# Performance work log

Hardware: AMD Instinct MI355X
Metric: run time of the kernel (lower is better)

## Reference

```python
import jax, jax.numpy as jnp
import numpy as np
import math

B, N, C = 8, 4096, 768
H = 12
DH = C // H
M = 256
LN_EPS = 1e-5


def setup_inputs() -> dict:
    key = jax.random.key(0)
    ks = jax.random.split(key, 7)
    x = jax.random.normal(ks[0], (B, N, C), dtype=jnp.float32)
    # torch Linear weight [out,in]; store transposed for y = x @ W
    W_qkv = jax.random.normal(ks[1], (C, 3 * C), dtype=jnp.float32) * (1.0 / math.sqrt(C))
    W_proj = jax.random.normal(ks[2], (C, C), dtype=jnp.float32) * (1.0 / math.sqrt(C))
    b_proj = jnp.zeros((C,), dtype=jnp.float32)
    gamma = jnp.ones((C,), dtype=jnp.float32)
    beta = jnp.zeros((C,), dtype=jnp.float32)
    random_features = jax.random.normal(ks[3], (M, DH), dtype=jnp.float32) / math.sqrt(DH)
    return {"x": x, "W_qkv": W_qkv, "W_proj": W_proj, "b_proj": b_proj,
            "gamma": gamma, "beta": beta, "random_features": random_features}


def _phi(t, random_features):
    # t: [B, H, N, DH] -> [B, H, N, M]; phi(x) = exp(w·x - ||x||^2/2) / sqrt(M)
    norm_sq = 0.5 * jnp.sum(t * t, axis=-1, keepdims=True)
    proj = jnp.einsum('bhnd,md->bhnm', t, random_features)
    return jnp.exp(proj - norm_sq) * (1.0 / math.sqrt(M))


def reference(x, W_qkv, W_proj, b_proj, gamma, beta, random_features):
    b, n, c = x.shape
    qkv = (x @ W_qkv).reshape(b, n, 3, H, DH)
    qkv = jnp.transpose(qkv, (2, 0, 3, 1, 4))  # [3, B, H, N, DH]
    q, k, v = qkv[0], qkv[1], qkv[2]

    q_p = _phi(q, random_features)  # [B,H,N,M]
    k_p = _phi(k, random_features)  # [B,H,N,M]

    kv = jnp.einsum('bhnm,bhnd->bhmd', k_p, v)       # [B,H,M,DH]
    out = jnp.einsum('bhnm,bhmd->bhnd', q_p, kv)     # [B,H,N,DH]

    k_sum = jnp.sum(k_p, axis=2)                      # [B,H,M]
    normalizer = jnp.einsum('bhnm,bhm->bhn', q_p, k_sum)[..., None]
    out = out / (normalizer + 1e-6)

    x_attn = jnp.transpose(out, (0, 2, 1, 3)).reshape(b, n, c)
    x_attn = x_attn @ W_proj + b_proj
    # dropout is identity in eval / p=0

    y = x + x_attn
    mu = jnp.mean(y, axis=-1, keepdims=True)
    var = jnp.mean(jnp.square(y - mu), axis=-1, keepdims=True)
    return (y - mu) * jax.lax.rsqrt(var + LN_EPS) * gamma + beta
```

## Files before the change

kernel.cpp:

```cpp
#include <hip/hip_runtime.h>
#include <hip/hip_fp16.h>


#define LOG2E 1.44269504088896340736f

typedef _Float16 half8 __attribute__((ext_vector_type(8)));
typedef _Float16 half4_t __attribute__((ext_vector_type(4)));
typedef _Float16 half2_t __attribute__((ext_vector_type(2)));
typedef float f32x4 __attribute__((ext_vector_type(4)));

#if __has_builtin(__builtin_amdgcn_fdot2)
#define FDOT2(a, b, c) __builtin_amdgcn_fdot2((a), (b), (c), false)
#else
#define FDOT2(a, b, c) \
  ((float)(a)[0] * (float)(b)[0] + ((float)(a)[1] * (float)(b)[1] + (c)))
#endif

static __device__ __forceinline__ half2_t pk2(float a, float b) {
#if __has_builtin(__builtin_amdgcn_cvt_pkrtz)
  return __builtin_bit_cast(half2_t, __builtin_amdgcn_cvt_pkrtz(a, b));
#else
  half2_t r; r[0] = (_Float16)a; r[1] = (_Float16)b; return r;
#endif
}

__device__ __forceinline__ void glds16(const _Float16* g, _Float16* s) {
  __builtin_amdgcn_global_load_lds(
      (const __attribute__((address_space(1))) void*)g,
      (__attribute__((address_space(3))) unsigned int*)s,
      16, 0, 0);
}


__global__ __launch_bounds__(256)
void prep(const float* __restrict__ x, const float* __restrict__ Wqkv,
          const float* __restrict__ Wproj, const float* __restrict__ rfm,
          _Float16* __restrict__ x_h, _Float16* __restrict__ wqkvT,
          _Float16* __restrict__ wprojT, _Float16* __restrict__ rfh) {
  const long bid = blockIdx.x;
  if (bid < 24576) {
    long i = (bid * 256 + threadIdx.x) * 4;
    float4 v = *(const float4*)(x + i);
    half4_t h;
    h[0] = (_Float16)v.x; h[1] = (_Float16)v.y; h[2] = (_Float16)v.z; h[3] = (_Float16)v.w;
    *(half4_t*)(x_h + i) = h;
    return;
  }
  long idx = (bid - 24576) * 256 + threadIdx.x;
  if (idx < 1769472) {
    int k = (int)(idx / 2304), n = (int)(idx % 2304);
    wqkvT[(long)n * 768 + k] = (_Float16)Wqkv[idx];
  } else if ((idx -= 1769472) < 589824) {
    int k = (int)(idx / 768), n = (int)(idx % 768);
    wprojT[(long)n * 768 + k] = (_Float16)Wproj[idx];
  } else if ((idx -= 589824) < 16384) {
    rfh[idx] = (_Float16)rfm[idx];
  }
}


__device__ __forceinline__ void stage_unit(const _Float16* __restrict__ G, int grow0,
                                           int kcol, _Float16* lds, int w, int l) {
#pragma unroll
  for (int j = 0; j < 2; ++j) {
    const int ci = w + j * 8;
    const int row = ci * 8 + (l >> 3);
    const int col8 = (l & 7) ^ (row & 7);
    glds16(G + (long)(grow0 + row) * 768 + kcol + col8 * 8, lds + ci * 512);
  }
}

static __device__ __forceinline__ half8 ldsw(const _Float16* buf, int r, int sl) {
  return *(const half8*)(buf + r * 64 + ((sl ^ (r & 7)) << 3));
}

__global__ __launch_bounds__(512)
void gemm_qkv(const _Float16* __restrict__ W, const _Float16* __restrict__ X,
              _Float16* __restrict__ qh, _Float16* __restrict__ kh,
              _Float16* __restrict__ vT,
              float* __restrict__ nsqLq, float* __restrict__ nsqLk) {
  __shared__ __align__(16) _Float16 As[32768];
  __shared__ __align__(16) _Float16 Bs[32768];
  const int tid = threadIdx.x;
  const int w = tid >> 6, l = tid & 63;
  const int lr = l & 15, kg = l >> 4;
  const int wr = w >> 2, wc = w & 3;

  const int bid = blockIdx.x;
  const int wg = (bid & 7) * 144 + (bid >> 3);
  const int m0 = (wg % 9) * 256;
  const int n0 = (wg / 9) * 256;

  stage_unit(W, m0,       0,  As,         w, l);
  stage_unit(X, n0,       0,  Bs,         w, l);
  stage_unit(X, n0 + 128, 0,  Bs + 8192,  w, l);
  stage_unit(W, m0 + 128, 0,  As + 8192,  w, l);
  stage_unit(W, m0,       64, As + 16384, w, l);
  stage_unit(X, n0,       64, Bs + 16384, w, l);
  stage_unit(X, n0 + 128, 64, Bs + 24576, w, l);
  asm volatile("s_waitcnt vmcnt(6)" ::: "memory");
  __builtin_amdgcn_s_barrier();

  f32x4 acc[8][4];
#pragma unroll
  for (int t = 0; t < 8; ++t)
#pragma unroll
    for (int u = 0; u < 4; ++u) acc[t][u] = (f32x4){0.f, 0.f, 0.f, 0.f};

  for (int kt = 0; kt < 12; ++kt) {
    const int c = kt & 1, o = c ^ 1;
    const _Float16* Ac = As + c * 16384;
    const _Float16* Bc = Bs + c * 16384;
    half8 aR[4][2], bR0[2][2], bR1[2][2];

#pragma unroll
    for (int i = 0; i < 4; ++i) {
      const int r = wr * 16 + i * 32 + lr;
      aR[i][0] = ldsw(Ac, r, kg);
      aR[i][1] = ldsw(Ac, r, 4 + kg);
    }
#pragma unroll
    for (int j = 0; j < 2; ++j) {
      const int r = wc * 16 + j * 64 + lr;
      bR0[j][0] = ldsw(Bc, r, kg);
      bR0[j][1] = ldsw(Bc, r, 4 + kg);
    }
    if (kt + 1 < 12)
      stage_unit(W, m0 + 128, (kt + 1) * 64, As + o * 16384 + 8192, w, l);
    __builtin_amdgcn_s_barrier();
    __builtin_amdgcn_s_setprio(1);
#pragma unroll
    for (int ks = 0; ks < 2; ++ks)
#pragma unroll
      for (int i = 0; i < 4; ++i)
#pragma unroll
        for (int j = 0; j < 2; ++j)
          acc[i][j] = __builtin_amdgcn_mfma_f32_16x16x32_f16(aR[i][ks], bR0[j][ks],
                                                             acc[i][j], 0, 0, 0);
    __builtin_amdgcn_s_setprio(0);
    __builtin_amdgcn_s_barrier();

#pragma unroll
    for (int j = 0; j < 2; ++j) {
      const int r = 128 + wc * 16 + j * 64 + lr;
      bR1[j][0] = ldsw(Bc, r, kg);
      bR1[j][1] = ldsw(Bc, r, 4 + kg);
    }
    if (kt + 2 < 12)
      stage_unit(W, m0, (kt + 2) * 64, As + c * 16384, w, l);
    __builtin_amdgcn_s_barrier();
    __builtin_amdgcn_s_setprio(1);
#pragma unroll
    for (int ks = 0; ks < 2; ++ks)
#pragma unroll
      for (int i = 0; i < 4; ++i)
#pragma unroll
        for (int j = 0; j < 2; ++j)
          acc[i][2 + j] = __builtin_amdgcn_mfma_f32_16x16x32_f16(aR[i][ks], bR1[j][ks],
                                                                 acc[i][2 + j], 0, 0, 0);
    __builtin_amdgcn_s_setprio(0);
    __builtin_amdgcn_s_barrier();

#pragma unroll
    for (int i = 0; i < 4; ++i) {
      const int r = 128 + wr * 16 + i * 32 + lr;
      aR[i][0] = ldsw(Ac, r, kg);
      aR[i][1] = ldsw(Ac, r, 4 + kg);
    }
    if (kt + 2 < 12)
      stage_unit(X, n0, (kt + 2) * 64, Bs + c * 16384, w, l);
    __builtin_amdgcn_s_barrier();
    __builtin_amdgcn_s_setprio(1);
#pragma unroll
    for (int ks = 0; ks < 2; ++ks)
#pragma unroll
      for (int i = 0; i < 4; ++i)
#pragma unroll
        for (int j = 0; j < 2; ++j)
          acc[4 + i][2 + j] = __builtin_amdgcn_mfma_f32_16x16x32_f16(aR[i][ks], bR1[j][ks],
                                                                     acc[4 + i][2 + j], 0, 0, 0);
    __builtin_amdgcn_s_setprio(0);
    __builtin_amdgcn_s_barrier();

    if (kt + 2 < 12)
      stage_unit(X, n0 + 128, (kt + 2) * 64, Bs + c * 16384 + 8192, w, l);
    if (kt < 10)
      asm volatile("s_waitcnt vmcnt(6)" ::: "memory");
    else
      asm volatile("s_waitcnt vmcnt(0)" ::: "memory");
    __builtin_amdgcn_s_barrier();
    __builtin_amdgcn_s_setprio(1);
#pragma unroll
    for (int ks = 0; ks < 2; ++ks)
#pragma unroll
      for (int i = 0; i < 4; ++i)
#pragma unroll
        for (int j = 0; j < 2; ++j)
          acc[4 + i][j] = __builtin_amdgcn_mfma_f32_16x16x32_f16(aR[i][ks], bR0[j][ks],
                                                                 acc[4 + i][j], 0, 0, 0);
    __builtin_amdgcn_s_setprio(0);
    __builtin_amdgcn_s_barrier();
  }

  const int which = (m0 >= 1536) ? 2 : ((m0 >= 768) ? 1 : 0);
  const int hbase = (m0 - which * 768) >> 6;
  const int b_ = n0 >> 12;
  const int nb = n0 & 4095;

  if (which < 2) {
    _Float16* dst = which ? kh : qh;
    float* nd = which ? nsqLk : nsqLq;
    float ns[4][4];
#pragma unroll
    for (int a = 0; a < 4; ++a)
#pragma unroll
      for (int b2 = 0; b2 < 4; ++b2) ns[a][b2] = 0.f;
#pragma unroll
    for (int t = 0; t < 8; ++t) {
      const int h = hbase + (t >> 1);
      const int d0 = wr * 16 + (t & 1) * 32 + kg * 4;
#pragma unroll
      for (int u = 0; u < 4; ++u) {
        const int n_ = nb + wc * 16 + u * 64 + lr;
        half2_t h01 = pk2(acc[t][u][0], acc[t][u][1]);
        half2_t h23 = pk2(acc[t][u][2], acc[t][u][3]);
        half4_t p4; p4[0] = h01[0]; p4[1] = h01[1]; p4[2] = h23[0]; p4[3] = h23[1];
        *(half4_t*)(dst + ((long)(b_ * 12 + h) * 4096 + n_) * 64 + d0) = p4;
#pragma unroll
        for (int r = 0; r < 4; ++r) { float f = (float)p4[r]; ns[t >> 1][u] += f * f; }
      }
    }
    float* nsP = (float*)As;
#pragma unroll
    for (int h2 = 0; h2 < 4; ++h2)
#pragma unroll
      for (int u = 0; u < 4; ++u) {
        float s = ns[h2][u];
        s += __shfl_xor(s, 16);
        s += __shfl_xor(s, 32);
        if (kg == 0) nsP[wr * 1024 + h2 * 256 + wc * 16 + u * 64 + lr] = s;
      }
    __syncthreads();
#pragma unroll
    for (int e = 0; e < 2; ++e) {
      const int idx = tid + e * 512;
      const int h2 = idx >> 8, tk = idx & 255;
      const float vsum = nsP[h2 * 256 + tk] + nsP[1024 + h2 * 256 + tk];
      nd[(long)(b_ * 12 + hbase + h2) * 4096 + nb + tk] = 0.5f * vsum * LOG2E + 4.0f;
    }
  } else {
#pragma unroll
    for (int t = 0; t < 8; ++t) {
      const int h = hbase + (t >> 1);
      const long hb = (long)(b_ * 12 + h) * 64;
      const int d0 = wr * 16 + (t & 1) * 32 + kg * 4;
#pragma unroll
      for (int u = 0; u < 4; ++u) {
        const int n_ = nb + wc * 16 + u * 64 + lr;
#pragma unroll
        for (int r = 0; r < 4; ++r)
          vT[(hb + d0 + r) * 4096 + n_] = (_Float16)acc[t][u][r];
      }
    }
  }
}


__global__ __launch_bounds__(256)
void gemm_proj(const _Float16* __restrict__ A, const _Float16* __restrict__ BT,
               float* __restrict__ Co, const float* __restrict__ bias,
               const float* __restrict__ resid) {
  __shared__ __align__(16) _Float16 As[128 * 32];
  __shared__ __align__(16) _Float16 Bs[128 * 32];
  const int tid = threadIdx.x;
  const int w = tid >> 6, l = tid & 63;
  const int lr = l & 15, kg = l >> 4;
  const int m0 = blockIdx.y * 128;
  const int n0 = blockIdx.x * 128;
  const int wm = (w >> 1) * 64, wn = (w & 1) * 64;

  const _Float16* gA = A + (long)(m0 + w * 32 + (l >> 2)) * 768 + (l & 3) * 8;
  const _Float16* gB = BT + (long)(n0 + w * 32 + (l >> 2)) * 768 + (l & 3) * 8;
  _Float16* sA = As + (w * 32) * 32;
  _Float16* sB = Bs + (w * 32) * 32;

  f32x4 acc[4][4];
#pragma unroll
  for (int t = 0; t < 4; ++t)
#pragma unroll
    for (int u = 0; u < 4; ++u) acc[t][u] = (f32x4){0.f, 0.f, 0.f, 0.f};

  for (int kc = 0; kc < 24; ++kc) {
    __syncthreads();
    glds16(gA, sA);
    glds16(gA + 16 * 768, sA + 16 * 32);
    glds16(gB, sB);
    glds16(gB + 16 * 768, sB + 16 * 32);
    gA += 32; gB += 32;
    __syncthreads();

    half8 af[4], bf[4];
#pragma unroll
    for (int t = 0; t < 4; ++t)
      af[t] = *(const half8*)(As + (wm + t * 16 + lr) * 32 + kg * 8);
#pragma unroll
    for (int u = 0; u < 4; ++u)
      bf[u] = *(const half8*)(Bs + (wn + u * 16 + lr) * 32 + kg * 8);
#pragma unroll
    for (int t = 0; t < 4; ++t)
#pragma unroll
      for (int u = 0; u < 4; ++u)
        acc[t][u] = __builtin_amdgcn_mfma_f32_16x16x32_f16(af[t], bf[u], acc[t][u], 0, 0, 0);
  }

#pragma unroll
  for (int u = 0; u < 4; ++u) {
    const int col = n0 + wn + u * 16 + lr;
    const float bv = bias[col];
#pragma unroll
    for (int t = 0; t < 4; ++t) {
      const int row = m0 + wm + t * 16 + kg * 4;
#pragma unroll
      for (int r = 0; r < 4; ++r) {
        long idx = (long)(row + r) * 768 + col;
        Co[idx] = acc[t][u][r] + bv + resid[idx];
      }
    }
  }
}


__global__ __launch_bounds__(256)
void kv_fused(const _Float16* __restrict__ kh, const _Float16* __restrict__ vT,
              const _Float16* __restrict__ rfh, const float* __restrict__ nsqLk,
              _Float16* __restrict__ kvpart, float* __restrict__ kspart) {
  __shared__ __align__(16) _Float16 Ka[64 * 32], Kb[64 * 32];
  __shared__ __align__(16) _Float16 Va[64 * 32], Vb[64 * 32];
  __shared__ __align__(16) _Float16 P[256 * 72];
  const int chunk = blockIdx.x, bh = blockIdx.y;
  const int tid = threadIdx.x, w = tid >> 6, l = tid & 63;
  const int lr = l & 15, kg = l >> 4;
  const long khbase = (long)bh * 4096 * 64;
  const long vtbase = (long)bh * 64 * 4096;
  const half2_t ONES = {(_Float16)1.f, (_Float16)1.f};

  half8 rf[4][2];
#pragma unroll
  for (int u = 0; u < 4; ++u)
#pragma unroll
    for (int ks = 0; ks < 2; ++ks)
      rf[u][ks] = *(const half8*)(rfh + (w * 64 + u * 16 + lr) * 64 + ks * 32 + kg * 8);

  f32x4 kvacc[4][4];
#pragma unroll
  for (int mt = 0; mt < 4; ++mt)
#pragma unroll
    for (int dt = 0; dt < 4; ++dt) kvacc[mt][dt] = (f32x4){0.f, 0.f, 0.f, 0.f};
  float ksacc[4] = {0.f, 0.f, 0.f, 0.f};

  for (int t8 = 0; t8 < 8; ++t8) {
    const int nt = chunk * 512 + t8 * 64;
    __syncthreads();
    if (w == 0) {
#pragma unroll
      for (int j = 0; j < 4; ++j)
        glds16(kh + khbase + (long)(nt + j * 16 + (l >> 2)) * 64 + (l & 3) * 8, Ka + j * 512);
    } else if (w == 1) {
#pragma unroll
      for (int j = 0; j < 4; ++j)
        glds16(kh + khbase + (long)(nt + j * 16 + (l >> 2)) * 64 + 32 + (l & 3) * 8, Kb + j * 512);
    } else if (w == 2) {
#pragma unroll
      for (int j = 0; j < 4; ++j)
        glds16(vT + vtbase + (long)(j * 16 + (l >> 2)) * 4096 + nt + (l & 3) * 8, Va + j * 512);
    } else {
#pragma unroll
      for (int j = 0; j < 4; ++j)
        glds16(vT + vtbase + (long)(j * 16 + (l >> 2)) * 4096 + nt + 32 + (l & 3) * 8, Vb + j * 512);
    }
    __syncthreads();

    half8 af[4][2];
#pragma unroll
    for (int tt = 0; tt < 4; ++tt) {
      af[tt][0] = *(const half8*)(Ka + (tt * 16 + lr) * 32 + kg * 8);
      af[tt][1] = *(const half8*)(Kb + (tt * 16 + lr) * 32 + kg * 8);
    }
    f32x4 sacc[4][4];
#pragma unroll
    for (int tt = 0; tt < 4; ++tt)
#pragma unroll
      for (int u = 0; u < 4; ++u) sacc[tt][u] = (f32x4){0.f, 0.f, 0.f, 0.f};
#pragma unroll
    for (int ks = 0; ks < 2; ++ks)
#pragma unroll
      for (int tt = 0; tt < 4; ++tt)
#pragma unroll
        for (int u = 0; u < 4; ++u)
          sacc[tt][u] = __builtin_amdgcn_mfma_f32_16x16x32_f16(af[tt][ks], rf[u][ks],
                                                               sacc[tt][u], 0, 0, 0);
    float4 nsq4[4];
#pragma unroll
    for (int tt = 0; tt < 4; ++tt)
      nsq4[tt] = *(const float4*)(nsqLk + (long)bh * 4096 + nt + tt * 16 + kg * 4);
#pragma unroll
    for (int tt = 0; tt < 4; ++tt)
#pragma unroll
      for (int u = 0; u < 4; ++u) {
        float e0 = exp2f(sacc[tt][u][0] * LOG2E - nsq4[tt].x);
        float e1 = exp2f(sacc[tt][u][1] * LOG2E - nsq4[tt].y);
        float e2 = exp2f(sacc[tt][u][2] * LOG2E - nsq4[tt].z);
        float e3 = exp2f(sacc[tt][u][3] * LOG2E - nsq4[tt].w);
        half2_t h01 = pk2(e0, e1), h23 = pk2(e2, e3);
        half4_t p4; p4[0] = h01[0]; p4[1] = h01[1]; p4[2] = h23[0]; p4[3] = h23[1];
        *(half4_t*)(P + (w * 64 + u * 16 + lr) * 72 + tt * 16 + kg * 4) = p4;
      }
#pragma unroll
    for (int ks = 0; ks < 2; ++ks) {
      half8 pa[4], bv[4];
#pragma unroll
      for (int mt = 0; mt < 4; ++mt)
        pa[mt] = *(const half8*)(P + (w * 64 + mt * 16 + lr) * 72 + ks * 32 + kg * 8);
#pragma unroll
      for (int dt = 0; dt < 4; ++dt)
        bv[dt] = *(const half8*)((ks == 0 ? Va : Vb) + (dt * 16 + lr) * 32 + kg * 8);
#pragma unroll
      for (int mt = 0; mt < 4; ++mt)
#pragma unroll
        for (int dt = 0; dt < 4; ++dt)
          kvacc[mt][dt] = __builtin_amdgcn_mfma_f32_16x16x32_f16(pa[mt], bv[dt],
                                                                 kvacc[mt][dt], 0, 0, 0);
#pragma unroll
      for (int mt = 0; mt < 4; ++mt) {
        const half2_t* pp = (const half2_t*)&pa[mt];
#pragma unroll
        for (int p = 0; p < 4; ++p) ksacc[mt] = FDOT2(pp[p], ONES, ksacc[mt]);
      }
    }
  }

#pragma unroll
  for (int mt = 0; mt < 4; ++mt) {
    float v = ksacc[mt];
    v += __shfl_xor(v, 16);
    v += __shfl_xor(v, 32);
    if (l < 16) kspart[((bh * 8 + chunk) << 8) + w * 64 + mt * 16 + l] = v;
  }
#pragma unroll
  for (int mt = 0; mt < 4; ++mt)
#pragma unroll
    for (int dt = 0; dt < 4; ++dt)
#pragma unroll
      for (int r = 0; r < 4; ++r)
        kvpart[(((long)(bh * 8 + chunk) * 256) + w * 64 + mt * 16 + kg * 4 + r) * 64 +
               dt * 16 + lr] = (_Float16)kvacc[mt][dt][r];
}


__global__ __launch_bounds__(256)
void reduce_all(const _Float16* __restrict__ kvpart, const float* __restrict__ kspart,
                _Float16* __restrict__ kvT, _Float16* __restrict__ ksumh) {
  if (blockIdx.x < 6144) {
    long i = (long)blockIdx.x * 256 + threadIdx.x;
    const int bh = (int)(i >> 14);
    const int rem = (int)(i & 16383);
    const int m = rem >> 6, d = rem & 63;
    float s = 0.f;
#pragma unroll
    for (int c = 0; c < 8; ++c)
      s += (float)kvpart[(((long)bh * 8 + c) * 256 + m) * 64 + d];
    kvT[(long)bh * 16384 + d * 256 + m] = (_Float16)s;
  } else {
    int i = (blockIdx.x - 6144) * 256 + threadIdx.x;
    int bh = i >> 8, m = i & 255;
    float s = 0.f;
#pragma unroll
    for (int c = 0; c < 8; ++c) s += kspart[((bh * 8 + c) << 8) + m];
    ksumh[i] = (_Float16)s;
  }
}


__global__ __launch_bounds__(256)
void attn_fused(const _Float16* __restrict__ qh, const _Float16* __restrict__ rfh,
                const float* __restrict__ nsqLq, const _Float16* __restrict__ kvT,
                const _Float16* __restrict__ ksumh, _Float16* __restrict__ attn) {
  __shared__ __align__(16) _Float16 Qa[64 * 32], Qb[64 * 32];
  __shared__ __align__(16) _Float16 KV[64 * 264];
  __shared__ __align__(16) _Float16 KS[256];
  __shared__ __align__(16) _Float16 P[64 * 264];
  __shared__ __align__(16) float NS[64];
  const int chunk = blockIdx.x, bh = blockIdx.y;
  const int b = bh / 12, h = bh % 12;
  const int tid = threadIdx.x, w = tid >> 6, l = tid & 63;
  const int lr = l & 15, kg = l >> 4;

  {
    const int d = tid >> 2, mb = (tid & 3) * 64;
#pragma unroll
    for (int j = 0; j < 8; ++j)
      *(half8*)(KV + d * 264 + mb + j * 8) =
          *(const half8*)(kvT + (long)bh * 16384 + d * 256 + mb + j * 8);
    if (tid < 32) *(half8*)(KS + tid * 8) = *(const half8*)(ksumh + bh * 256 + tid * 8);
  }

  half8 rf[4][2];
#pragma unroll
  for (int mt = 0; mt < 4; ++mt)
#pragma unroll
    for (int ks = 0; ks < 2; ++ks)
      rf[mt][ks] = *(const half8*)(rfh + (w * 64 + mt * 16 + lr) * 64 + ks * 32 + kg * 8);

  for (int t8 = 0; t8 < 4; ++t8) {
    const int nt = chunk * 256 + t8 * 64;
    __syncthreads();
    if (w == 0) {
#pragma unroll
      for (int j = 0; j < 4; ++j)
        glds16(qh + ((long)bh * 4096 + nt + j * 16 + (l >> 2)) * 64 + (l & 3) * 8, Qa + j * 512);
    } else if (w == 1) {
#pragma unroll
      for (int j = 0; j < 4; ++j)
        glds16(qh + ((long)bh * 4096 + nt + j * 16 + (l >> 2)) * 64 + 32 + (l & 3) * 8, Qb + j * 512);
    }
    __syncthreads();

    half8 bq[4][2];
#pragma unroll
    for (int tt = 0; tt < 4; ++tt) {
      bq[tt][0] = *(const half8*)(Qa + (tt * 16 + lr) * 32 + kg * 8);
      bq[tt][1] = *(const half8*)(Qb + (tt * 16 + lr) * 32 + kg * 8);
    }
    f32x4 sacc[4][4];
#pragma unroll
    for (int mt = 0; mt < 4; ++mt)
#pragma unroll
      for (int tt = 0; tt < 4; ++tt) sacc[mt][tt] = (f32x4){0.f, 0.f, 0.f, 0.f};
#pragma unroll
    for (int ks = 0; ks < 2; ++ks)
#pragma unroll
      for (int mt = 0; mt < 4; ++mt)
#pragma unroll
        for (int tt = 0; tt < 4; ++tt)
          sacc[mt][tt] = __builtin_amdgcn_mfma_f32_16x16x32_f16(rf[mt][ks], bq[tt][ks],
                                                                sacc[mt][tt], 0, 0, 0);
    float nsqv[4];
#pragma unroll
    for (int tt = 0; tt < 4; ++tt)
      nsqv[tt] = nsqLq[(long)bh * 4096 + nt + tt * 16 + lr];
#pragma unroll
    for (int mt = 0; mt < 4; ++mt)
#pragma unroll
      for (int tt = 0; tt < 4; ++tt) {
        float e0 = exp2f(sacc[mt][tt][0] * LOG2E - nsqv[tt]);
        float e1 = exp2f(sacc[mt][tt][1] * LOG2E - nsqv[tt]);
        float e2 = exp2f(sacc[mt][tt][2] * LOG2E - nsqv[tt]);
        float e3 = exp2f(sacc[mt][tt][3] * LOG2E - nsqv[tt]);
        half2_t h01 = pk2(e0, e1), h23 = pk2(e2, e3);
        half4_t p4; p4[0] = h01[0]; p4[1] = h01[1]; p4[2] = h23[0]; p4[3] = h23[1];
        *(half4_t*)(P + (tt * 16 + lr) * 264 + w * 64 + mt * 16 + kg * 4) = p4;
      }
    __syncthreads();

    f32x4 oacc[4];
#pragma unroll
    for (int u = 0; u < 4; ++u) oacc[u] = (f32x4){0.f, 0.f, 0.f, 0.f};
    float nacc = 0.f;
#pragma unroll
    for (int ks = 0; ks < 8; ++ks) {
      half8 ap = *(const half8*)(P + (w * 16 + lr) * 264 + ks * 32 + kg * 8);
      half8 kv8 = *(const half8*)(KS + ks * 32 + kg * 8);
      const half2_t* a2 = (const half2_t*)&ap;
      const half2_t* k2 = (const half2_t*)&kv8;
#pragma unroll
      for (int p = 0; p < 4; ++p) nacc = FDOT2(a2[p], k2[p], nacc);
#pragma unroll
      for (int u = 0; u < 4; ++u) {
        half8 bkv = *(const half8*)(KV + (u * 16 + lr) * 264 + ks * 32 + kg * 8);
        oacc[u] = __builtin_amdgcn_mfma_f32_16x16x32_f16(ap, bkv, oacc[u], 0, 0, 0);
      }
    }
    nacc += __shfl_xor(nacc, 16);
    nacc += __shfl_xor(nacc, 32);
    if (l < 16) NS[w * 16 + l] = nacc;
    f32x4 n4 = *(const f32x4*)(NS + w * 16 + kg * 4);
    float inv[4];
#pragma unroll
    for (int r = 0; r < 4; ++r) inv[r] = 1.f / (n4[r] + 1e-6f);
#pragma unroll
    for (int u = 0; u < 4; ++u)
#pragma unroll
      for (int r = 0; r < 4; ++r)
        attn[((long)b * 4096 + nt + w * 16 + kg * 4 + r) * 768 + h * 64 + u * 16 + lr] =
            (_Float16)(oacc[u][r] * inv[r]);
  }
}


__global__ __launch_bounds__(256)
void ln_kernel(const float* __restrict__ y, const float* __restrict__ gamma,
               const float* __restrict__ beta, float* __restrict__ outp) {
  const int wv = threadIdx.x >> 6, l = threadIdx.x & 63;
  const long row = (long)blockIdx.x * 4 + wv;
  const float* yr = y + row * 768;
  float v[12];
  float s = 0.f;
#pragma unroll
  for (int j = 0; j < 12; ++j) { v[j] = yr[l + j * 64]; s += v[j]; }
#pragma unroll
  for (int off = 32; off; off >>= 1) s += __shfl_xor(s, off);
  const float mu = s * (1.f / 768.f);
  float vs = 0.f;
#pragma unroll
  for (int j = 0; j < 12; ++j) { float d = v[j] - mu; vs += d * d; }
#pragma unroll
  for (int off = 32; off; off >>= 1) vs += __shfl_xor(vs, off);
  const float rstd = rsqrtf(vs * (1.f / 768.f) + 1e-5f);
  float* orp = outp + row * 768;
#pragma unroll
  for (int j = 0; j < 12; ++j)
    orp[l + j * 64] = (v[j] - mu) * rstd * gamma[l + j * 64] + beta[l + j * 64];
}


extern "C" void kernel_launch(void* const* d_in, const int* in_sizes, int n_in,
                              void* d_out, int out_size, void* d_ws, size_t ws_size,
                              hipStream_t stream) {
  const float* x = (const float*)d_in[0];
  const float* Wqkv = (const float*)d_in[1];
  const float* Wproj = (const float*)d_in[2];
  const float* bproj = (const float*)d_in[3];
  const float* gamma = (const float*)d_in[4];
  const float* beta = (const float*)d_in[5];
  const float* rfm = (const float*)d_in[6];

  char* ws = (char*)d_ws;
  size_t off = 0;
  auto alloc = [&](size_t bytes) -> void* {
    void* p = ws + off;
    off += (bytes + 255) & ~(size_t)255;
    return p;
  };
  char* regionA = (char*)alloc(50331648ULL);
  _Float16* x_h = (_Float16*)regionA;
  _Float16* kvpart = (_Float16*)regionA;
  _Float16* attn = (_Float16*)regionA;

  _Float16* wqkvT = (_Float16*)alloc(1769472ULL * 2);
  _Float16* wprojT = (_Float16*)alloc(589824ULL * 2);
  _Float16* rfh = (_Float16*)alloc(16384ULL * 2);
  _Float16* qh = (_Float16*)alloc(25165824ULL * 2);
  _Float16* kh = (_Float16*)alloc(25165824ULL * 2);
  _Float16* vT = (_Float16*)alloc(25165824ULL * 2);
  float* nsqLq = (float*)alloc(393216ULL * 4);
  float* nsqLk = (float*)alloc(393216ULL * 4);
  float* kspart = (float*)alloc(96ULL * 8 * 256 * 4);
  _Float16* kvT = (_Float16*)alloc(96ULL * 16384 * 2);
  _Float16* ksumh = (_Float16*)alloc(96ULL * 256 * 2);

  float* y = (float*)d_out;

  prep<<<33856, 256, 0, stream>>>(x, Wqkv, Wproj, rfm, x_h, wqkvT, wprojT, rfh);
  gemm_qkv<<<1152, 512, 0, stream>>>(wqkvT, x_h, qh, kh, vT, nsqLq, nsqLk);
  kv_fused<<<dim3(8, 96), 256, 0, stream>>>(kh, vT, rfh, nsqLk, kvpart, kspart);
  reduce_all<<<6240, 256, 0, stream>>>(kvpart, kspart, kvT, ksumh);
  attn_fused<<<dim3(16, 96), 256, 0, stream>>>(qh, rfh, nsqLq, kvT, ksumh, attn);
  gemm_proj<<<dim3(6, 256), 256, 0, stream>>>(attn, wprojT, y, bproj, x);
  ln_kernel<<<8192, 256, 0, stream>>>(y, gamma, beta, y);
}
```

Before: 612.9 us.

## Tile weight transpose through LDS and prefetch next k-tile GEMM fragments

The prep kernel now transposes Wqkv and Wproj in 64x64 tiles through shared memory, giving coalesced float4 reads and half8 writes in place of strided scalar stores, and it launches far fewer blocks. The QKV GEMM main loop is reordered so the A and B fragments for the next k-tile are loaded from the other LDS buffer during the last MFMA phase, and each phase's fragment loads are rearranged. This aims to hide LDS read latency behind MFMA work, at the cost of more live vector registers, which may lower occupancy.

Measured after the change: 648.4 us. +5.8%, slower.

```diff
diff --git a/kernel.cpp b/kernel.cpp
--- a/kernel.cpp
+++ b/kernel.cpp
@@ -37,24 +37,47 @@
           const float* __restrict__ Wproj, const float* __restrict__ rfm,
           _Float16* __restrict__ x_h, _Float16* __restrict__ wqkvT,
           _Float16* __restrict__ wprojT, _Float16* __restrict__ rfh) {
-  const long bid = blockIdx.x;
+  __shared__ _Float16 T[64][72];
+  const int bid = blockIdx.x;
   if (bid < 24576) {
-    long i = (bid * 256 + threadIdx.x) * 4;
+    long i = ((long)bid * 256 + threadIdx.x) * 4;
     float4 v = *(const float4*)(x + i);
     half4_t h;
     h[0] = (_Float16)v.x; h[1] = (_Float16)v.y; h[2] = (_Float16)v.z; h[3] = (_Float16)v.w;
     *(half4_t*)(x_h + i) = h;
     return;
   }
-  long idx = (bid - 24576) * 256 + threadIdx.x;
-  if (idx < 1769472) {
-    int k = (int)(idx / 2304), n = (int)(idx % 2304);
-    wqkvT[(long)n * 768 + k] = (_Float16)Wqkv[idx];
-  } else if ((idx -= 1769472) < 589824) {
-    int k = (int)(idx / 768), n = (int)(idx % 768);
-    wprojT[(long)n * 768 + k] = (_Float16)Wproj[idx];
-  } else if ((idx -= 589824) < 16384) {
-    rfh[idx] = (_Float16)rfm[idx];
+  int tb = bid - 24576;
+  if (tb < 576) {
+    const float* src; _Float16* dst; int Csrc, r0, c0;
+    if (tb < 432) {
+      r0 = (tb / 36) * 64; c0 = (tb % 36) * 64; src = Wqkv; dst = wqkvT; Csrc = 2304;
+    } else {
+      int t2 = tb - 432;
+      r0 = (t2 / 12) * 64; c0 = (t2 % 12) * 64; src = Wproj; dst = wprojT; Csrc = 768;
+    }
+    const int ri = threadIdx.x >> 4;
+    const int ci = (threadIdx.x & 15) * 4;
+#pragma unroll
+    for (int rr = 0; rr < 4; ++rr) {
+      float4 v = *(const float4*)(src + (long)(r0 + ri * 4 + rr) * Csrc + c0 + ci);
+      T[ci + 0][ri * 4 + rr] = (_Float16)v.x;
+      T[ci + 1][ri * 4 + rr] = (_Float16)v.y;
+      T[ci + 2][ri * 4 + rr] = (_Float16)v.z;
+      T[ci + 3][ri * 4 + rr] = (_Float16)v.w;
+    }
+    __syncthreads();
+    const int wi = threadIdx.x >> 3;
+    const int wj = (threadIdx.x & 7) * 8;
+#pragma unroll
+    for (int ww = 0; ww < 2; ++ww) {
+      const int row = wi * 2 + ww;
+      half8 h = *(const half8*)(&T[row][wj]);
+      *(half8*)(dst + (long)(c0 + row) * 768 + r0 + wj) = h;
+    }
+  } else {
+    int idx = (tb - 576) * 256 + threadIdx.x;
+    if (idx < 16384) rfh[idx] = (_Float16)rfm[idx];
   }
 }
 
@@ -107,23 +130,32 @@
 #pragma unroll
     for (int u = 0; u < 4; ++u) acc[t][u] = (f32x4){0.f, 0.f, 0.f, 0.f};
 
+  half8 a0[4][2], a1[4][2], b0[2][2], b1[2][2], b0n[2][2];
+#pragma unroll
+  for (int i = 0; i < 4; ++i) {
+    const int r = wr * 16 + i * 32 + lr;
+    a0[i][0] = ldsw(As, r, kg);
+    a0[i][1] = ldsw(As, r, 4 + kg);
+  }
+#pragma unroll
+  for (int j = 0; j < 2; ++j) {
+    const int r = wc * 16 + j * 64 + lr;
+    b0[j][0] = ldsw(Bs, r, kg);
+    b0[j][1] = ldsw(Bs, r, 4 + kg);
+  }
+
   for (int kt = 0; kt < 12; ++kt) {
     const int c = kt & 1, o = c ^ 1;
     const _Float16* Ac = As + c * 16384;
     const _Float16* Bc = Bs + c * 16384;
-    half8 aR[4][2], bR0[2][2], bR1[2][2];
-
-#pragma unroll
-    for (int i = 0; i < 4; ++i) {
-      const int r = wr * 16 + i * 32 + lr;
-      aR[i][0] = ldsw(Ac, r, kg);
-      aR[i][1] = ldsw(Ac, r, 4 + kg);
-    }
+    const _Float16* An = As + o * 16384;
+    const _Float16* Bn = Bs + o * 16384;
+
 #pragma unroll
     for (int j = 0; j < 2; ++j) {
-      const int r = wc * 16 + j * 64 + lr;
-      bR0[j][0] = ldsw(Bc, r, kg);
-      bR0[j][1] = ldsw(Bc, r, 4 + kg);
+      const int r = 128 + wc * 16 + j * 64 + lr;
+      b1[j][0] = ldsw(Bc, r, kg);
+      b1[j][1] = ldsw(Bc, r, 4 + kg);
     }
     if (kt + 1 < 12)
       stage_unit(W, m0 + 128, (kt + 1) * 64, As + o * 16384 + 8192, w, l);
@@ -135,16 +167,16 @@
       for (int i = 0; i < 4; ++i)
 #pragma unroll
         for (int j = 0; j < 2; ++j)
-          acc[i][j] = __builtin_amdgcn_mfma_f32_16x16x32_f16(aR[i][ks], bR0[j][ks],
+          acc[i][j] = __builtin_amdgcn_mfma_f32_16x16x32_f16(a0[i][ks], b0[j][ks],
                                                              acc[i][j], 0, 0, 0);
     __builtin_amdgcn_s_setprio(0);
     __builtin_amdgcn_s_barrier();
 
 #pragma unroll
-    for (int j = 0; j < 2; ++j) {
-      const int r = 128 + wc * 16 + j * 64 + lr;
-      bR1[j][0] = ldsw(Bc, r, kg);
-      bR1[j][1] = ldsw(Bc, r, 4 + kg);
+    for (int i = 0; i < 4; ++i) {
+      const int r = 128 + wr * 16 + i * 32 + lr;
+      a1[i][0] = ldsw(Ac, r, kg);
+      a1[i][1] = ldsw(Ac, r, 4 + kg);
     }
     if (kt + 2 < 12)
       stage_unit(W, m0, (kt + 2) * 64, As + c * 16384, w, l);
@@ -156,17 +188,11 @@
       for (int i = 0; i < 4; ++i)
 #pragma unroll
         for (int j = 0; j < 2; ++j)
-          acc[i][2 + j] = __builtin_amdgcn_mfma_f32_16x16x32_f16(aR[i][ks], bR1[j][ks],
+          acc[i][2 + j] = __builtin_amdgcn_mfma_f32_16x16x32_f16(a0[i][ks], b1[j][ks],
                                                                  acc[i][2 + j], 0, 0, 0);
     __builtin_amdgcn_s_setprio(0);
     __builtin_amdgcn_s_barrier();
 
-#pragma unroll
-    for (int i = 0; i < 4; ++i) {
-      const int r = 128 + wr * 16 + i * 32 + lr;
-      aR[i][0] = ldsw(Ac, r, kg);
-      aR[i][1] = ldsw(Ac, r, 4 + kg);
-    }
     if (kt + 2 < 12)
       stage_unit(X, n0, (kt + 2) * 64, Bs + c * 16384, w, l);
     __builtin_amdgcn_s_barrier();
@@ -177,7 +203,7 @@
       for (int i = 0; i < 4; ++i)
 #pragma unroll
         for (int j = 0; j < 2; ++j)
-          acc[4 + i][2 + j] = __builtin_amdgcn_mfma_f32_16x16x32_f16(aR[i][ks], bR1[j][ks],
+          acc[4 + i][2 + j] = __builtin_amdgcn_mfma_f32_16x16x32_f16(a1[i][ks], b1[j][ks],
                                                                      acc[4 + i][2 + j], 0, 0, 0);
     __builtin_amdgcn_s_setprio(0);
     __builtin_amdgcn_s_barrier();
@@ -188,6 +214,20 @@
       asm volatile("s_waitcnt vmcnt(6)" ::: "memory");
     else
       asm volatile("s_waitcnt vmcnt(0)" ::: "memory");
+    if (kt + 1 < 12) {
+#pragma unroll
+      for (int i = 0; i < 4; ++i) {
+        const int r = wr * 16 + i * 32 + lr;
+        a0[i][0] = ldsw(An, r, kg);
+        a0[i][1] = ldsw(An, r, 4 + kg);
+      }
+#pragma unroll
+      for (int j = 0; j < 2; ++j) {
+        const int r = wc * 16 + j * 64 + lr;
+        b0n[j][0] = ldsw(Bn, r, kg);
+        b0n[j][1] = ldsw(Bn, r, 4 + kg);
+      }
+    }
     __builtin_amdgcn_s_barrier();
     __builtin_amdgcn_s_setprio(1);
 #pragma unroll
@@ -196,10 +236,14 @@
       for (int i = 0; i < 4; ++i)
 #pragma unroll
         for (int j = 0; j < 2; ++j)
-          acc[4 + i][j] = __builtin_amdgcn_mfma_f32_16x16x32_f16(aR[i][ks], bR0[j][ks],
+          acc[4 + i][j] = __builtin_amdgcn_mfma_f32_16x16x32_f16(a1[i][ks], b0[j][ks],
                                                                  acc[4 + i][j], 0, 0, 0);
     __builtin_amdgcn_s_setprio(0);
     __builtin_amdgcn_s_barrier();
+    if (kt + 1 < 12) {
+#pragma unroll
+      for (int j = 0; j < 2; ++j) { b0[j][0] = b0n[j][0]; b0[j][1] = b0n[j][1]; }
+    }
   }
 
   const int which = (m0 >= 1536) ? 2 : ((m0 >= 768) ? 1 : 0);
@@ -660,7 +704,7 @@
 
   float* y = (float*)d_out;
 
-  prep<<<33856, 256, 0, stream>>>(x, Wqkv, Wproj, rfm, x_h, wqkvT, wprojT, rfh);
+  prep<<<25216, 256, 0, stream>>>(x, Wqkv, Wproj, rfm, x_h, wqkvT, wprojT, rfh);
   gemm_qkv<<<1152, 512, 0, stream>>>(wqkvT, x_h, qh, kh, vT, nsqLq, nsqLk);
   kv_fused<<<dim3(8, 96), 256, 0, stream>>>(kh, vT, rfh, nsqLk, kvpart, kspart);
   reduce_all<<<6240, 256, 0, stream>>>(kvpart, kspart, kvT, ksumh);
```
